# Optimization experiments

Measured on AMD Instinct MI355X. Metric: run time of the kernel, lower is better.

Reference implementation:

```python
import jax, jax.numpy as jnp
import numpy as np

FP8_E4M3_MAX = 448.0
FP4_E2M1_MAX = 6.0
BLOCK = 16  # NVFP4 block-scale granularity


def _round_e4m3(x):
    """Round non-negative values to fp8 e4m3 grid (3 mantissa bits, min normal 2^-6, max 448)."""
    a = jnp.abs(x)
    e = jnp.clip(jnp.floor(jnp.log2(jnp.where(a > 0, a, 1.0))), -6.0, 8.0)
    s = jnp.exp2(e)
    q = jnp.round(a / s * 8.0) / 8.0 * s
    q = jnp.clip(q, 0.0, FP8_E4M3_MAX)
    return jnp.where(a > 0, q, 0.0)


def _round_e2m1(x):
    """Round to fp4 e2m1 grid: +/- {0, 0.5, 1, 1.5, 2, 3, 4, 6}."""
    sgn = jnp.sign(x)
    a = jnp.clip(jnp.abs(x), 0.0, FP4_E2M1_MAX)
    e = jnp.clip(jnp.floor(jnp.log2(jnp.where(a > 0, a, 1.0))), 0.0, 2.0)
    step = jnp.exp2(e) * 0.5  # 0.5 in [0,2), 1 in [2,4), 2 in [4,6]
    q = jnp.round(a / step) * step
    return sgn * jnp.clip(q, 0.0, FP4_E2M1_MAX)


def quant_nvfp4(t):
    """Dynamic NVFP4 quantization (vLLM scaled_fp4_quant semantics).
    Returns (q_fp4 [R, K/16, 16], block_scale_e4m3 [R, K/16], global_scale []).
    Dequant: q * block_scale / global_scale."""
    gs = (FP8_E4M3_MAX * FP4_E2M1_MAX) / jnp.max(jnp.abs(t))
    tb = t.reshape(t.shape[0], -1, BLOCK)
    block_amax = jnp.max(jnp.abs(tb), axis=-1)              # [R, K/16]
    bs = _round_e4m3(block_amax / FP4_E2M1_MAX * gs)         # e4m3 block scales
    safe_bs = jnp.where(bs > 0, bs, 1.0)
    q = _round_e2m1(tb * (gs / safe_bs)[..., None])
    q = jnp.where((bs > 0)[..., None], q, 0.0)
    return q, bs, gs


def setup_inputs() -> dict:
    key = jax.random.key(0)
    kx, kw = jax.random.split(key)
    tokens, hidden = 8192, 4096
    x = jax.random.normal(kx, (tokens, 2 * hidden), dtype=jnp.float32)
    w = jax.random.uniform(kw, (hidden, hidden), dtype=jnp.float32)
    return {"x": x, "w": w}


def reference(x, w):
    d = x.shape[-1] // 2
    # SiluAndMul
    y = jax.nn.silu(x[..., :d]) * x[..., d:]                # [T, H]
    # dynamic NVFP4 quant of activation and weight
    qy, sy, gy = quant_nvfp4(y)
    qw, sw, gw = quant_nvfp4(w)
    # cutlass_scaled_fp4_mm: out = (qy*sy) @ (qw*sw)^T * alpha, alpha = 1/(gy*gw)
    a = (qy * sy[..., None]).reshape(y.shape)               # [T, H]
    b = (qw * sw[..., None]).reshape(w.shape)               # [H, H]
    alpha = 1.0 / (gy * gw)
    return (a @ b.T) * alpha
```

## Files before the change

### kernel.cpp

```cpp
#include <hip/hip_runtime.h>
#include <hip/hip_bf16.h>

typedef __attribute__((ext_vector_type(8))) short bf16x8;
typedef __attribute__((ext_vector_type(4))) float f32x4;


__device__ __forceinline__ float silu_mul_f(float a, float b) {
  float s = 1.0f / (1.0f + expf(-a));
  return (a * s) * b;
}

__device__ __forceinline__ int flog2(float a) {
  return (int)((__float_as_uint(a) >> 23) & 255u) - 127;
}
__device__ __forceinline__ float exp2i(int e) {
  return __uint_as_float((unsigned)(e + 127) << 23);
}

__device__ __forceinline__ float round_e4m3_f(float a) {
  if (!(a > 0.0f)) return 0.0f;
  int e = flog2(a);
  e = e < -6 ? -6 : (e > 8 ? 8 : e);
  float q = rintf(a * exp2i(3 - e)) * exp2i(e - 3);
  return fminf(q, 448.0f);
}

__device__ __forceinline__ float round_e2m1_f(float x) {
  float a = fminf(fabsf(x), 6.0f);
  if (!(a > 0.0f)) return 0.0f;
  int e = flog2(a);
  e = e < 0 ? 0 : (e > 2 ? 2 : e);
  float q = rintf(a * exp2i(1 - e)) * exp2i(e - 1);
  q = fminf(q, 6.0f);
  return (x < 0.0f) ? -q : q;
}

__global__ void init_scal_kernel(float* scal) {
  if (threadIdx.x < 2) scal[threadIdx.x] = 0.0f;
}


__global__ void amax2_kernel(const float* __restrict__ x, const float* __restrict__ w,
                             float* __restrict__ scal, long actU, long wU,
                             int hidden, int hqLog) {
  float mA = 0.0f, mW = 0.0f;
  const long stride = (long)gridDim.x * blockDim.x;
  const long hqm = (1L << hqLog) - 1;
  const long total = actU + wU;
  for (long u = (long)blockIdx.x * blockDim.x + threadIdx.x; u < total; u += stride) {
    if (u < actU) {
      long row = u >> hqLog;
      long c = u & hqm;
      const float* xr = x + ((row * (long)hidden) << 1);
      float4 v1 = ((const float4*)xr)[c];
      float4 v2 = ((const float4*)(xr + hidden))[c];
      mA = fmaxf(mA, fabsf(silu_mul_f(v1.x, v2.x)));
      mA = fmaxf(mA, fabsf(silu_mul_f(v1.y, v2.y)));
      mA = fmaxf(mA, fabsf(silu_mul_f(v1.z, v2.z)));
      mA = fmaxf(mA, fabsf(silu_mul_f(v1.w, v2.w)));
    } else {
      float4 v = ((const float4*)w)[u - actU];
      mW = fmaxf(mW, fmaxf(fmaxf(fabsf(v.x), fabsf(v.y)), fmaxf(fabsf(v.z), fabsf(v.w))));
    }
  }
#pragma unroll
  for (int off = 32; off > 0; off >>= 1) {
    mA = fmaxf(mA, __shfl_xor(mA, off));
    mW = fmaxf(mW, __shfl_xor(mW, off));
  }
  __shared__ float sA[4], sW[4];
  if ((threadIdx.x & 63) == 0) { sA[threadIdx.x >> 6] = mA; sW[threadIdx.x >> 6] = mW; }
  __syncthreads();
  if (threadIdx.x == 0) {
    atomicMax((unsigned int*)(scal + 0),
              __float_as_uint(fmaxf(fmaxf(sA[0], sA[1]), fmaxf(sA[2], sA[3]))));
    atomicMax((unsigned int*)(scal + 1),
              __float_as_uint(fmaxf(fmaxf(sW[0], sW[1]), fmaxf(sW[2], sW[3]))));
  }
}


__global__ void quant2_kernel(const float* __restrict__ x, const float* __restrict__ w,
                              __hip_bfloat16* __restrict__ A, __hip_bfloat16* __restrict__ B,
                              const float* __restrict__ scal, long actU, long wU,
                              int hidden, int hqLog) {
  const float gsA = 2688.0f / scal[0];
  const float gsW = 2688.0f / scal[1];
  const long stride = (long)gridDim.x * blockDim.x;
  const long hqm = (1L << hqLog) - 1;
  const long total = actU + wU;
  for (long u = (long)blockIdx.x * blockDim.x + threadIdx.x; u < total; u += stride) {
    float y0, y1, y2, y3, gs;
    unsigned short* dst;
    if (u < actU) {
      long row = u >> hqLog;
      long c = u & hqm;
      const float* xr = x + ((row * (long)hidden) << 1) + (c << 2);
      float4 v1 = *(const float4*)xr;
      float4 v2 = *(const float4*)(xr + hidden);
      y0 = silu_mul_f(v1.x, v2.x);
      y1 = silu_mul_f(v1.y, v2.y);
      y2 = silu_mul_f(v1.z, v2.z);
      y3 = silu_mul_f(v1.w, v2.w);
      gs = gsA;
      dst = (unsigned short*)A + (u << 2);
    } else {
      float4 v = ((const float4*)w)[u - actU];
      y0 = v.x; y1 = v.y; y2 = v.z; y3 = v.w;
      gs = gsW;
      dst = (unsigned short*)B + ((u - actU) << 2);
    }
    float lm = fmaxf(fmaxf(fabsf(y0), fabsf(y1)), fmaxf(fabsf(y2), fabsf(y3)));
    lm = fmaxf(lm, __shfl_xor(lm, 1));
    lm = fmaxf(lm, __shfl_xor(lm, 2));
    float bs = round_e4m3_f(lm / 6.0f * gs);
    float r = gs / (bs > 0.0f ? bs : 1.0f);
    ushort4 o;
    o.x = (unsigned short)(__float_as_uint(round_e2m1_f(y0 * r) * bs) >> 16);
    o.y = (unsigned short)(__float_as_uint(round_e2m1_f(y1 * r) * bs) >> 16);
    o.z = (unsigned short)(__float_as_uint(round_e2m1_f(y2 * r) * bs) >> 16);
    o.w = (unsigned short)(__float_as_uint(round_e2m1_f(y3 * r) * bs) >> 16);
    *(ushort4*)dst = o;
  }
}


__device__ __forceinline__ void gload_lds16(const void* g, void* l) {
  __builtin_amdgcn_global_load_lds(
      (const __attribute__((address_space(1))) void*)(uintptr_t)g,
      (__attribute__((address_space(3))) void*)(uintptr_t)l, 16, 0, 0);
}

template <unsigned IMM>
__device__ __forceinline__ bf16x8 lds_read16o(unsigned addr) {
  bf16x8 r;
  asm volatile("ds_read_b128 %0, %1 offset:%c2" : "=&v"(r) : "v"(addr), "i"(IMM));
  return r;
}

__device__ __forceinline__ f32x4 mfma_(bf16x8 a, bf16x8 b, f32x4 c) {
  return __builtin_amdgcn_mfma_f32_16x16x32_bf16(a, b, c, 0, 0, 0);
}

#define SP1 __builtin_amdgcn_s_setprio(1)
#define SP0 __builtin_amdgcn_s_setprio(0)
#define SCHEDB __builtin_amdgcn_sched_barrier(0)
#define WAITL(n) do { asm volatile("s_waitcnt lgkmcnt(" #n ")" ::: "memory"); SCHEDB; } while (0)
#define VMW4 do { asm volatile("s_waitcnt vmcnt(4)" ::: "memory"); } while (0)

#define STAGEA(PP, HH, KSB) do {                                        \
    const char* _s = pa + (KSB) + (HH) * 64;                            \
    gload_lds16(_s, ldsStA + (PP) * 32768 + (HH) * 16384);              \
    gload_lds16(_s + rowBig, ldsStA + (PP) * 32768 + (HH) * 16384 + 8192); } while (0)

#define STAGEB(PP, HH, KSB) do {                                        \
    const char* _s = pb + (KSB) + (HH) * 64;                            \
    gload_lds16(_s, ldsStB + (PP) * 32768 + (HH) * 16384);              \
    gload_lds16(_s + rowBig, ldsStB + (PP) * 32768 + (HH) * 16384 + 8192); } while (0)

#define RDA4(DST, PP, HH, MB) do {                                              \
    DST[0] = lds_read16o<(PP)*32768u + (HH)*16384u + ((MB)+0)*1024u>(vA);       \
    DST[1] = lds_read16o<(PP)*32768u + (HH)*16384u + ((MB)+1)*1024u>(vA);       \
    DST[2] = lds_read16o<(PP)*32768u + (HH)*16384u + ((MB)+2)*1024u>(vA);       \
    DST[3] = lds_read16o<(PP)*32768u + (HH)*16384u + ((MB)+3)*1024u>(vA); } while (0)

#define RDB4(DST, PP, HH) do {                                                  \
    DST[0] = lds_read16o<(PP)*32768u + (HH)*16384u + 0u>(vB);                   \
    DST[1] = lds_read16o<(PP)*32768u + (HH)*16384u + 1024u>(vB);                \
    DST[2] = lds_read16o<(PP)*32768u + (HH)*16384u + 2048u>(vB);                \
    DST[3] = lds_read16o<(PP)*32768u + (HH)*16384u + 3072u>(vB); } while (0)

#define MFMA16(AF, BF, MB) do {                                                  \
    acc[(MB)+0][0] = mfma_(AF[0], BF[0], acc[(MB)+0][0]);                        \
    acc[(MB)+1][0] = mfma_(AF[1], BF[0], acc[(MB)+1][0]);                        \
    acc[(MB)+2][0] = mfma_(AF[2], BF[0], acc[(MB)+2][0]);                        \
    acc[(MB)+3][0] = mfma_(AF[3], BF[0], acc[(MB)+3][0]);                        \
    acc[(MB)+0][1] = mfma_(AF[0], BF[1], acc[(MB)+0][1]);                        \
    acc[(MB)+1][1] = mfma_(AF[1], BF[1], acc[(MB)+1][1]);                        \
    acc[(MB)+2][1] = mfma_(AF[2], BF[1], acc[(MB)+2][1]);                        \
    acc[(MB)+3][1] = mfma_(AF[3], BF[1], acc[(MB)+3][1]);                        \
    acc[(MB)+0][2] = mfma_(AF[0], BF[2], acc[(MB)+0][2]);                        \
    acc[(MB)+1][2] = mfma_(AF[1], BF[2], acc[(MB)+1][2]);                        \
    acc[(MB)+2][2] = mfma_(AF[2], BF[2], acc[(MB)+2][2]);                        \
    acc[(MB)+3][2] = mfma_(AF[3], BF[2], acc[(MB)+3][2]);                        \
    acc[(MB)+0][3] = mfma_(AF[0], BF[3], acc[(MB)+0][3]);                        \
    acc[(MB)+1][3] = mfma_(AF[1], BF[3], acc[(MB)+1][3]);                        \
    acc[(MB)+2][3] = mfma_(AF[2], BF[3], acc[(MB)+2][3]);                        \
    acc[(MB)+3][3] = mfma_(AF[3], BF[3], acc[(MB)+3][3]); } while (0)

#define TILE(P, KSB) do {                                                        \
    STAGEA((P)^1, 0, KSB);                                                       \
    RDA4(aY, P, 0, 4);                                                           \
    WAITL(4);                                                                    \
    SP1; MFMA16(aX, bb0, 0); SP0;                                                \
    STAGEB((P)^1, 0, KSB);                                                       \
    VMW4;                                                                        \
    __builtin_amdgcn_s_barrier(); SCHEDB;                                        \
    RDA4(aX, P, 1, 0); RDB4(bb1, P, 1);                                          \
    WAITL(8);                                                                    \
    SP1; MFMA16(aY, bb0, 4); SP0;                                                \
    STAGEA((P)^1, 1, KSB);                                                       \
    RDA4(aY, P, 1, 4);                                                           \
    WAITL(4);                                                                    \
    SP1; MFMA16(aX, bb1, 0); SP0;                                                \
    STAGEB((P)^1, 1, KSB);                                                       \
    WAITL(0);                                                                    \
    VMW4;                                                                        \
    __builtin_amdgcn_s_barrier(); SCHEDB;                                        \
    RDA4(aX, (P)^1, 0, 0); RDB4(bb0, (P)^1, 0); SCHEDB;                          \
    SP1; MFMA16(aY, bb1, 4); SP0;                                                \
  } while (0)

__global__ __launch_bounds__(512, 2) void gemm_bt_kernel(
    const __hip_bfloat16* __restrict__ A, const __hip_bfloat16* __restrict__ B,
    float* __restrict__ C, const float* __restrict__ scal, int M, int N, int K) {
  __shared__ __align__(16) char lds[131072];

  const int nbm = M >> 8, nbn = N >> 8;
  int wg = blockIdx.x, bm, bn;
  if ((nbm & 7) == 0) {
    int band = nbm >> 3;
    int xcd = wg & 7, c = wg >> 3;
    bm = xcd * band + (c % band);
    bn = c / band;
  } else {
    bm = wg / nbn; bn = wg % nbn;
  }
  const int brow = bm << 8, bcol = bn << 8;

  const int tid = threadIdx.x;
  const int lane = tid & 63;
  const int wave = tid >> 6;
  const int wm = wave >> 2, wn = wave & 3;

  const int srow = tid >> 2;
  const int slc = (tid & 3) ^ ((tid >> 3) & 3);
  const char* pa = (const char*)(A + (size_t)(brow + srow) * K + slc * 8);
  const char* pb = (const char*)(B + (size_t)(bcol + srow) * K + slc * 8);
  const size_t rowBig = (size_t)128 * K * 2;
  char* ldsStA = lds + tid * 16;
  char* ldsStB = lds + 65536 + tid * 16;

  const unsigned ldsBase = (unsigned)(uintptr_t)lds;
  const unsigned xoff = (unsigned)((lane & 15) * 64) +
                        ((((unsigned)(lane >> 4)) ^ (((unsigned)lane >> 1) & 3u)) << 4);
  const unsigned vA = ldsBase + (unsigned)(wm * 8192) + xoff;
  const unsigned vB = ldsBase + 65536u + (unsigned)(wn * 4096) + xoff;

  f32x4 acc[8][4] = {};
  bf16x8 aX[4], aY[4], bb0[4], bb1[4];

  STAGEA(0, 0, 0); STAGEB(0, 0, 0); STAGEA(0, 1, 0); STAGEB(0, 1, 0);
  asm volatile("s_waitcnt vmcnt(0)" ::: "memory");
  __syncthreads();
  RDA4(aX, 0, 0, 0); RDB4(bb0, 0, 0); SCHEDB;

  const int nt = K >> 6;
  for (int it = 0; it < (nt >> 1); ++it) {
    int t0 = it << 1;
    int ks0 = (t0 + 1) * 128;
    int ks1 = (t0 + 2 == nt) ? 0 : (t0 + 2) * 128;
    TILE(0, ks0);
    TILE(1, ks1);
  }
  asm volatile("s_waitcnt lgkmcnt(0)" ::: "memory");
  asm volatile("s_waitcnt vmcnt(0)" ::: "memory");

  float gy = 2688.0f / scal[0];
  float gw = 2688.0f / scal[1];
  float alpha = 1.0f / (gy * gw);

#pragma unroll
  for (int m = 0; m < 8; ++m) {
    int rbase = brow + wm * 128 + m * 16 + ((lane >> 4) << 2);
#pragma unroll
    for (int n = 0; n < 4; ++n) {
      int col = bcol + wn * 64 + n * 16 + (lane & 15);
#pragma unroll
      for (int rg = 0; rg < 4; ++rg) {
        C[(size_t)(rbase + rg) * N + col] = acc[m][n][rg] * alpha;
      }
    }
  }
}


extern "C" void kernel_launch(void* const* d_in, const int* in_sizes, int n_in,
                              void* d_out, int out_size, void* d_ws, size_t ws_size,
                              hipStream_t stream) {
  const float* x = (const float*)d_in[0];
  const float* w = (const float*)d_in[1];
  float* out = (float*)d_out;

  int hidden = 1;
  while ((long long)hidden * hidden < (long long)in_sizes[1]) hidden <<= 1;
  int tokens = in_sizes[0] / (2 * hidden);

  char* ws = (char*)d_ws;
  __hip_bfloat16* Aq = (__hip_bfloat16*)ws;
  __hip_bfloat16* Bq = (__hip_bfloat16*)(ws + (size_t)tokens * hidden * 2);
  float* scal = (float*)(ws + (size_t)tokens * hidden * 2 + (size_t)hidden * hidden * 2);

  long actU = (long)tokens * hidden / 4;
  long wU = (long)hidden * hidden / 4;
  int hqLog = __builtin_ctz((unsigned)(hidden >> 2));

  init_scal_kernel<<<1, 64, 0, stream>>>(scal);
  amax2_kernel<<<2048, 256, 0, stream>>>(x, w, scal, actU, wU, hidden, hqLog);
  quant2_kernel<<<2048, 256, 0, stream>>>(x, w, Aq, Bq, scal, actU, wU, hidden, hqLog);

  int grid = (tokens >> 8) * (hidden >> 8);
  gemm_bt_kernel<<<grid, 512, 0, stream>>>(Aq, Bq, out, scal, tokens, hidden, hidden);
}
```

Measured before the change: 414.0 us.

## Switch GEMM to 32x32x16 MFMA and split quant kernels by tensor

The GEMM inner loop now uses 32x32x16 bf16 MFMA tiles with 16-float accumulators in place of 16x16x32. This halves the number of MFMA issues and LDS fragment reads per tile, with new swizzled LDS read addresses and a new epilogue layout. The amax and quant kernels now assign dedicated block ranges to activation and weight, which removes the per-element branch. Their loops are also unrolled by two to keep more loads in flight. The changed fragment addressing risks bank conflicts or wrong output layout if the swizzle math is off.

After: 395.5 us. 1.05x faster.

```diff
diff --git a/kernel.cpp b/kernel.cpp
--- a/kernel.cpp
+++ b/kernel.cpp
@@ -3,6 +3,7 @@
 
 typedef __attribute__((ext_vector_type(8))) short bf16x8;
 typedef __attribute__((ext_vector_type(4))) float f32x4;
+typedef __attribute__((ext_vector_type(16))) float f32x16;
 
 
 __device__ __forceinline__ float silu_mul_f(float a, float b) {
@@ -40,87 +41,125 @@
 }
 
 
+__device__ __forceinline__ float act_unit_max(const float* __restrict__ x, long u,
+                                              int hidden, long hqm, int hqLog) {
+  long row = u >> hqLog, c = u & hqm;
+  const float* xr = x + ((row * (long)hidden) << 1);
+  float4 v1 = ((const float4*)xr)[c];
+  float4 v2 = ((const float4*)(xr + hidden))[c];
+  float m = fmaxf(fabsf(silu_mul_f(v1.x, v2.x)), fabsf(silu_mul_f(v1.y, v2.y)));
+  m = fmaxf(m, fmaxf(fabsf(silu_mul_f(v1.z, v2.z)), fabsf(silu_mul_f(v1.w, v2.w))));
+  return m;
+}
+
 __global__ void amax2_kernel(const float* __restrict__ x, const float* __restrict__ w,
                              float* __restrict__ scal, long actU, long wU,
-                             int hidden, int hqLog) {
-  float mA = 0.0f, mW = 0.0f;
-  const long stride = (long)gridDim.x * blockDim.x;
+                             int hidden, int hqLog, int AB) {
   const long hqm = (1L << hqLog) - 1;
-  const long total = actU + wU;
-  for (long u = (long)blockIdx.x * blockDim.x + threadIdx.x; u < total; u += stride) {
-    if (u < actU) {
-      long row = u >> hqLog;
-      long c = u & hqm;
-      const float* xr = x + ((row * (long)hidden) << 1);
-      float4 v1 = ((const float4*)xr)[c];
-      float4 v2 = ((const float4*)(xr + hidden))[c];
-      mA = fmaxf(mA, fabsf(silu_mul_f(v1.x, v2.x)));
-      mA = fmaxf(mA, fabsf(silu_mul_f(v1.y, v2.y)));
-      mA = fmaxf(mA, fabsf(silu_mul_f(v1.z, v2.z)));
-      mA = fmaxf(mA, fabsf(silu_mul_f(v1.w, v2.w)));
-    } else {
-      float4 v = ((const float4*)w)[u - actU];
-      mW = fmaxf(mW, fmaxf(fmaxf(fabsf(v.x), fabsf(v.y)), fmaxf(fabsf(v.z), fabsf(v.w))));
-    }
-  }
-#pragma unroll
-  for (int off = 32; off > 0; off >>= 1) {
-    mA = fmaxf(mA, __shfl_xor(mA, off));
-    mW = fmaxf(mW, __shfl_xor(mW, off));
-  }
-  __shared__ float sA[4], sW[4];
-  if ((threadIdx.x & 63) == 0) { sA[threadIdx.x >> 6] = mA; sW[threadIdx.x >> 6] = mW; }
+  float m = 0.0f;
+  int which;
+  if ((int)blockIdx.x < AB) {
+    which = 0;
+    const long stride = (long)AB * blockDim.x;
+    long u = (long)blockIdx.x * blockDim.x + threadIdx.x;
+    for (; u + stride < actU; u += 2 * stride) {
+      float m0 = act_unit_max(x, u, hidden, hqm, hqLog);
+      float m1 = act_unit_max(x, u + stride, hidden, hqm, hqLog);
+      m = fmaxf(m, fmaxf(m0, m1));
+    }
+    if (u < actU) m = fmaxf(m, act_unit_max(x, u, hidden, hqm, hqLog));
+  } else {
+    which = 1;
+    const long stride = (long)(gridDim.x - AB) * blockDim.x;
+    long u = (long)((int)blockIdx.x - AB) * blockDim.x + threadIdx.x;
+    for (; u + stride < wU; u += 2 * stride) {
+      float4 v1 = ((const float4*)w)[u];
+      float4 v2 = ((const float4*)w)[u + stride];
+      float m0 = fmaxf(fmaxf(fabsf(v1.x), fabsf(v1.y)), fmaxf(fabsf(v1.z), fabsf(v1.w)));
+      float m1 = fmaxf(fmaxf(fabsf(v2.x), fabsf(v2.y)), fmaxf(fabsf(v2.z), fabsf(v2.w)));
+      m = fmaxf(m, fmaxf(m0, m1));
+    }
+    if (u < wU) {
+      float4 v = ((const float4*)w)[u];
+      m = fmaxf(m, fmaxf(fmaxf(fabsf(v.x), fabsf(v.y)), fmaxf(fabsf(v.z), fabsf(v.w))));
+    }
+  }
+#pragma unroll
+  for (int off = 32; off > 0; off >>= 1) m = fmaxf(m, __shfl_xor(m, off));
+  __shared__ float sm[4];
+  if ((threadIdx.x & 63) == 0) sm[threadIdx.x >> 6] = m;
   __syncthreads();
   if (threadIdx.x == 0) {
-    atomicMax((unsigned int*)(scal + 0),
-              __float_as_uint(fmaxf(fmaxf(sA[0], sA[1]), fmaxf(sA[2], sA[3]))));
-    atomicMax((unsigned int*)(scal + 1),
-              __float_as_uint(fmaxf(fmaxf(sW[0], sW[1]), fmaxf(sW[2], sW[3]))));
-  }
-}
-
+    float mm = fmaxf(fmaxf(sm[0], sm[1]), fmaxf(sm[2], sm[3]));
+    atomicMax((unsigned int*)(scal + which), __float_as_uint(mm));
+  }
+}
+
+
+__device__ __forceinline__ void quant_unit(float y0, float y1, float y2, float y3,
+                                           float gs, unsigned short* dst) {
+  float lm = fmaxf(fmaxf(fabsf(y0), fabsf(y1)), fmaxf(fabsf(y2), fabsf(y3)));
+  lm = fmaxf(lm, __shfl_xor(lm, 1));
+  lm = fmaxf(lm, __shfl_xor(lm, 2));
+  float bs = round_e4m3_f(lm / 6.0f * gs);
+  float r = gs / (bs > 0.0f ? bs : 1.0f);
+  ushort4 o;
+  o.x = (unsigned short)(__float_as_uint(round_e2m1_f(y0 * r) * bs) >> 16);
+  o.y = (unsigned short)(__float_as_uint(round_e2m1_f(y1 * r) * bs) >> 16);
+  o.z = (unsigned short)(__float_as_uint(round_e2m1_f(y2 * r) * bs) >> 16);
+  o.w = (unsigned short)(__float_as_uint(round_e2m1_f(y3 * r) * bs) >> 16);
+  *(ushort4*)dst = o;
+}
 
 __global__ void quant2_kernel(const float* __restrict__ x, const float* __restrict__ w,
                               __hip_bfloat16* __restrict__ A, __hip_bfloat16* __restrict__ B,
                               const float* __restrict__ scal, long actU, long wU,
-                              int hidden, int hqLog) {
-  const float gsA = 2688.0f / scal[0];
-  const float gsW = 2688.0f / scal[1];
-  const long stride = (long)gridDim.x * blockDim.x;
+                              int hidden, int hqLog, int AB) {
   const long hqm = (1L << hqLog) - 1;
-  const long total = actU + wU;
-  for (long u = (long)blockIdx.x * blockDim.x + threadIdx.x; u < total; u += stride) {
-    float y0, y1, y2, y3, gs;
-    unsigned short* dst;
+  if ((int)blockIdx.x < AB) {
+    const float gs = 2688.0f / scal[0];
+    const long stride = (long)AB * blockDim.x;
+    long u = (long)blockIdx.x * blockDim.x + threadIdx.x;
+    for (; u + stride < actU; u += 2 * stride) {
+      long ua = u, ub = u + stride;
+      long ra = ua >> hqLog, ca = ua & hqm;
+      long rb = ub >> hqLog, cb = ub & hqm;
+      const float* xa = x + ((ra * (long)hidden) << 1) + (ca << 2);
+      const float* xb = x + ((rb * (long)hidden) << 1) + (cb << 2);
+      float4 a1 = *(const float4*)xa;
+      float4 a2 = *(const float4*)(xa + hidden);
+      float4 b1 = *(const float4*)xb;
+      float4 b2 = *(const float4*)(xb + hidden);
+      quant_unit(silu_mul_f(a1.x, a2.x), silu_mul_f(a1.y, a2.y),
+                 silu_mul_f(a1.z, a2.z), silu_mul_f(a1.w, a2.w),
+                 gs, (unsigned short*)A + (ua << 2));
+      quant_unit(silu_mul_f(b1.x, b2.x), silu_mul_f(b1.y, b2.y),
+                 silu_mul_f(b1.z, b2.z), silu_mul_f(b1.w, b2.w),
+                 gs, (unsigned short*)A + (ub << 2));
+    }
     if (u < actU) {
-      long row = u >> hqLog;
       long c = u & hqm;
-      const float* xr = x + ((row * (long)hidden) << 1) + (c << 2);
-      float4 v1 = *(const float4*)xr;
-      float4 v2 = *(const float4*)(xr + hidden);
-      y0 = silu_mul_f(v1.x, v2.x);
-      y1 = silu_mul_f(v1.y, v2.y);
-      y2 = silu_mul_f(v1.z, v2.z);
-      y3 = silu_mul_f(v1.w, v2.w);
-      gs = gsA;
-      dst = (unsigned short*)A + (u << 2);
-    } else {
-      float4 v = ((const float4*)w)[u - actU];
-      y0 = v.x; y1 = v.y; y2 = v.z; y3 = v.w;
-      gs = gsW;
-      dst = (unsigned short*)B + ((u - actU) << 2);
-    }
-    float lm = fmaxf(fmaxf(fabsf(y0), fabsf(y1)), fmaxf(fabsf(y2), fabsf(y3)));
-    lm = fmaxf(lm, __shfl_xor(lm, 1));
-    lm = fmaxf(lm, __shfl_xor(lm, 2));
-    float bs = round_e4m3_f(lm / 6.0f * gs);
-    float r = gs / (bs > 0.0f ? bs : 1.0f);
-    ushort4 o;
-    o.x = (unsigned short)(__float_as_uint(round_e2m1_f(y0 * r) * bs) >> 16);
-    o.y = (unsigned short)(__float_as_uint(round_e2m1_f(y1 * r) * bs) >> 16);
-    o.z = (unsigned short)(__float_as_uint(round_e2m1_f(y2 * r) * bs) >> 16);
-    o.w = (unsigned short)(__float_as_uint(round_e2m1_f(y3 * r) * bs) >> 16);
-    *(ushort4*)dst = o;
+      const float* xa = x + (((u >> hqLog) * (long)hidden) << 1) + (c << 2);
+      float4 v1 = *(const float4*)xa;
+      float4 v2 = *(const float4*)(xa + hidden);
+      quant_unit(silu_mul_f(v1.x, v2.x), silu_mul_f(v1.y, v2.y),
+                 silu_mul_f(v1.z, v2.z), silu_mul_f(v1.w, v2.w),
+                 gs, (unsigned short*)A + (u << 2));
+    }
+  } else {
+    const float gs = 2688.0f / scal[1];
+    const long stride = (long)(gridDim.x - AB) * blockDim.x;
+    long u = (long)((int)blockIdx.x - AB) * blockDim.x + threadIdx.x;
+    for (; u + stride < wU; u += 2 * stride) {
+      float4 v1 = ((const float4*)w)[u];
+      float4 v2 = ((const float4*)w)[u + stride];
+      quant_unit(v1.x, v1.y, v1.z, v1.w, gs, (unsigned short*)B + (u << 2));
+      quant_unit(v2.x, v2.y, v2.z, v2.w, gs, (unsigned short*)B + ((u + stride) << 2));
+    }
+    if (u < wU) {
+      float4 v = ((const float4*)w)[u];
+      quant_unit(v.x, v.y, v.z, v.w, gs, (unsigned short*)B + (u << 2));
+    }
   }
 }
 
@@ -138,8 +177,8 @@
   return r;
 }
 
-__device__ __forceinline__ f32x4 mfma_(bf16x8 a, bf16x8 b, f32x4 c) {
-  return __builtin_amdgcn_mfma_f32_16x16x32_bf16(a, b, c, 0, 0, 0);
+__device__ __forceinline__ f32x16 mfma32(bf16x8 a, bf16x8 b, f32x16 c) {
+  return __builtin_amdgcn_mfma_f32_32x32x16_bf16(a, b, c, 0, 0, 0);
 }
 
 #define SP1 __builtin_amdgcn_s_setprio(1)
@@ -158,57 +197,47 @@
     gload_lds16(_s, ldsStB + (PP) * 32768 + (HH) * 16384);              \
     gload_lds16(_s + rowBig, ldsStB + (PP) * 32768 + (HH) * 16384 + 8192); } while (0)
 
-#define RDA4(DST, PP, HH, MB) do {                                              \
-    DST[0] = lds_read16o<(PP)*32768u + (HH)*16384u + ((MB)+0)*1024u>(vA);       \
-    DST[1] = lds_read16o<(PP)*32768u + (HH)*16384u + ((MB)+1)*1024u>(vA);       \
-    DST[2] = lds_read16o<(PP)*32768u + (HH)*16384u + ((MB)+2)*1024u>(vA);       \
-    DST[3] = lds_read16o<(PP)*32768u + (HH)*16384u + ((MB)+3)*1024u>(vA); } while (0)
-
-#define RDB4(DST, PP, HH) do {                                                  \
-    DST[0] = lds_read16o<(PP)*32768u + (HH)*16384u + 0u>(vB);                   \
-    DST[1] = lds_read16o<(PP)*32768u + (HH)*16384u + 1024u>(vB);                \
-    DST[2] = lds_read16o<(PP)*32768u + (HH)*16384u + 2048u>(vB);                \
-    DST[3] = lds_read16o<(PP)*32768u + (HH)*16384u + 3072u>(vB); } while (0)
-
-#define MFMA16(AF, BF, MB) do {                                                  \
-    acc[(MB)+0][0] = mfma_(AF[0], BF[0], acc[(MB)+0][0]);                        \
-    acc[(MB)+1][0] = mfma_(AF[1], BF[0], acc[(MB)+1][0]);                        \
-    acc[(MB)+2][0] = mfma_(AF[2], BF[0], acc[(MB)+2][0]);                        \
-    acc[(MB)+3][0] = mfma_(AF[3], BF[0], acc[(MB)+3][0]);                        \
-    acc[(MB)+0][1] = mfma_(AF[0], BF[1], acc[(MB)+0][1]);                        \
-    acc[(MB)+1][1] = mfma_(AF[1], BF[1], acc[(MB)+1][1]);                        \
-    acc[(MB)+2][1] = mfma_(AF[2], BF[1], acc[(MB)+2][1]);                        \
-    acc[(MB)+3][1] = mfma_(AF[3], BF[1], acc[(MB)+3][1]);                        \
-    acc[(MB)+0][2] = mfma_(AF[0], BF[2], acc[(MB)+0][2]);                        \
-    acc[(MB)+1][2] = mfma_(AF[1], BF[2], acc[(MB)+1][2]);                        \
-    acc[(MB)+2][2] = mfma_(AF[2], BF[2], acc[(MB)+2][2]);                        \
-    acc[(MB)+3][2] = mfma_(AF[3], BF[2], acc[(MB)+3][2]);                        \
-    acc[(MB)+0][3] = mfma_(AF[0], BF[3], acc[(MB)+0][3]);                        \
-    acc[(MB)+1][3] = mfma_(AF[1], BF[3], acc[(MB)+1][3]);                        \
-    acc[(MB)+2][3] = mfma_(AF[2], BF[3], acc[(MB)+2][3]);                        \
-    acc[(MB)+3][3] = mfma_(AF[3], BF[3], acc[(MB)+3][3]); } while (0)
-
-#define TILE(P, KSB) do {                                                        \
-    STAGEA((P)^1, 0, KSB);                                                       \
-    RDA4(aY, P, 0, 4);                                                           \
-    WAITL(4);                                                                    \
-    SP1; MFMA16(aX, bb0, 0); SP0;                                                \
-    STAGEB((P)^1, 0, KSB);                                                       \
-    VMW4;                                                                        \
-    __builtin_amdgcn_s_barrier(); SCHEDB;                                        \
-    RDA4(aX, P, 1, 0); RDB4(bb1, P, 1);                                          \
-    WAITL(8);                                                                    \
-    SP1; MFMA16(aY, bb0, 4); SP0;                                                \
-    STAGEA((P)^1, 1, KSB);                                                       \
-    RDA4(aY, P, 1, 4);                                                           \
-    WAITL(4);                                                                    \
-    SP1; MFMA16(aX, bb1, 0); SP0;                                                \
-    STAGEB((P)^1, 1, KSB);                                                       \
-    WAITL(0);                                                                    \
-    VMW4;                                                                        \
-    __builtin_amdgcn_s_barrier(); SCHEDB;                                        \
-    RDA4(aX, (P)^1, 0, 0); RDB4(bb0, (P)^1, 0); SCHEDB;                          \
-    SP1; MFMA16(aY, bb1, 4); SP0;                                                \
+#define RDA(DST, PP, HH, KS) do {                                           \
+    DST[0] = lds_read16o<(PP)*32768u + (HH)*16384u + 0u>(vA##KS);           \
+    DST[1] = lds_read16o<(PP)*32768u + (HH)*16384u + 2048u>(vA##KS);        \
+    DST[2] = lds_read16o<(PP)*32768u + (HH)*16384u + 4096u>(vA##KS);        \
+    DST[3] = lds_read16o<(PP)*32768u + (HH)*16384u + 6144u>(vA##KS); } while (0)
+
+#define RDB(DST, PP, HH, KS) do {                                           \
+    DST[0] = lds_read16o<(PP)*32768u + (HH)*16384u + 0u>(vB##KS);           \
+    DST[1] = lds_read16o<(PP)*32768u + (HH)*16384u + 2048u>(vB##KS); } while (0)
+
+#define MFMA8(AF, BF) do {                               \
+    acc[0][0] = mfma32(AF[0], BF[0], acc[0][0]);         \
+    acc[1][0] = mfma32(AF[1], BF[0], acc[1][0]);         \
+    acc[2][0] = mfma32(AF[2], BF[0], acc[2][0]);         \
+    acc[3][0] = mfma32(AF[3], BF[0], acc[3][0]);         \
+    acc[0][1] = mfma32(AF[0], BF[1], acc[0][1]);         \
+    acc[1][1] = mfma32(AF[1], BF[1], acc[1][1]);         \
+    acc[2][1] = mfma32(AF[2], BF[1], acc[2][1]);         \
+    acc[3][1] = mfma32(AF[3], BF[1], acc[3][1]); } while (0)
+
+#define TILE(P, KSB) do {                                                \
+    STAGEA((P)^1, 0, KSB);                                               \
+    RDA(aB, P, 0, 1); RDB(bB, P, 0, 1);                                  \
+    WAITL(6);                                                            \
+    SP1; MFMA8(aA, bA); SP0;                                             \
+    STAGEB((P)^1, 0, KSB);                                               \
+    VMW4;                                                                \
+    __builtin_amdgcn_s_barrier(); SCHEDB;                                \
+    RDA(aA, P, 1, 0); RDB(bA, P, 1, 0);                                  \
+    WAITL(6);                                                            \
+    SP1; MFMA8(aB, bB); SP0;                                             \
+    STAGEA((P)^1, 1, KSB);                                               \
+    RDA(aB, P, 1, 1); RDB(bB, P, 1, 1);                                  \
+    WAITL(6);                                                            \
+    SP1; MFMA8(aA, bA); SP0;                                             \
+    STAGEB((P)^1, 1, KSB);                                               \
+    VMW4;                                                                \
+    __builtin_amdgcn_s_barrier(); SCHEDB;                                \
+    RDA(aA, (P)^1, 0, 0); RDB(bA, (P)^1, 0, 0);                          \
+    WAITL(6);                                                            \
+    SP1; MFMA8(aB, bB); SP0;                                             \
   } while (0)
 
 __global__ __launch_bounds__(512, 2) void gemm_bt_kernel(
@@ -242,18 +271,22 @@
   char* ldsStB = lds + 65536 + tid * 16;
 
   const unsigned ldsBase = (unsigned)(uintptr_t)lds;
-  const unsigned xoff = (unsigned)((lane & 15) * 64) +
-                        ((((unsigned)(lane >> 4)) ^ (((unsigned)lane >> 1) & 3u)) << 4);
-  const unsigned vA = ldsBase + (unsigned)(wm * 8192) + xoff;
-  const unsigned vB = ldsBase + 65536u + (unsigned)(wn * 4096) + xoff;
-
-  f32x4 acc[8][4] = {};
-  bf16x8 aX[4], aY[4], bb0[4], bb1[4];
+  const unsigned l31 = (unsigned)(lane & 31);
+  const unsigned half = (unsigned)(lane >> 5);
+  const unsigned sw = ((unsigned)lane >> 1) & 3u;
+  const unsigned rbyte = l31 * 64u;
+  const unsigned vA0 = ldsBase + (unsigned)(wm * 8192) + rbyte + ((half ^ sw) << 4);
+  const unsigned vA1 = ldsBase + (unsigned)(wm * 8192) + rbyte + (((2u + half) ^ sw) << 4);
+  const unsigned vB0 = ldsBase + 65536u + (unsigned)(wn * 4096) + rbyte + ((half ^ sw) << 4);
+  const unsigned vB1 = ldsBase + 65536u + (unsigned)(wn * 4096) + rbyte + (((2u + half) ^ sw) << 4);
+
+  f32x16 acc[4][2] = {};
+  bf16x8 aA[4], aB[4], bA[2], bB[2];
 
   STAGEA(0, 0, 0); STAGEB(0, 0, 0); STAGEA(0, 1, 0); STAGEB(0, 1, 0);
   asm volatile("s_waitcnt vmcnt(0)" ::: "memory");
   __syncthreads();
-  RDA4(aX, 0, 0, 0); RDB4(bb0, 0, 0); SCHEDB;
+  RDA(aA, 0, 0, 0); RDB(bA, 0, 0, 0); SCHEDB;
 
   const int nt = K >> 6;
   for (int it = 0; it < (nt >> 1); ++it) {
@@ -271,14 +304,17 @@
   float alpha = 1.0f / (gy * gw);
 
 #pragma unroll
-  for (int m = 0; m < 8; ++m) {
-    int rbase = brow + wm * 128 + m * 16 + ((lane >> 4) << 2);
-#pragma unroll
-    for (int n = 0; n < 4; ++n) {
-      int col = bcol + wn * 64 + n * 16 + (lane & 15);
-#pragma unroll
-      for (int rg = 0; rg < 4; ++rg) {
-        C[(size_t)(rbase + rg) * N + col] = acc[m][n][rg] * alpha;
+  for (int mf = 0; mf < 4; ++mf) {
+    int rb = brow + wm * 128 + mf * 32 + (int)(half << 2);
+#pragma unroll
+    for (int nf = 0; nf < 2; ++nf) {
+      int col = bcol + wn * 64 + nf * 32 + (int)l31;
+#pragma unroll
+      for (int g = 0; g < 4; ++g) {
+#pragma unroll
+        for (int r = 0; r < 4; ++r) {
+          C[(size_t)(rb + 8 * g + r) * N + col] = acc[mf][nf][g * 4 + r] * alpha;
+        }
       }
     }
   }
@@ -304,10 +340,15 @@
   long actU = (long)tokens * hidden / 4;
   long wU = (long)hidden * hidden / 4;
   int hqLog = __builtin_ctz((unsigned)(hidden >> 2));
+  int nBlk = 2048;
+  int AB = (int)(((long)nBlk * actU) / (actU + wU));
+  AB &= ~3;
+  if (AB < 1) AB = 1;
+  if (AB > nBlk - 1) AB = nBlk - 1;
 
   init_scal_kernel<<<1, 64, 0, stream>>>(scal);
-  amax2_kernel<<<2048, 256, 0, stream>>>(x, w, scal, actU, wU, hidden, hqLog);
-  quant2_kernel<<<2048, 256, 0, stream>>>(x, w, Aq, Bq, scal, actU, wU, hidden, hqLog);
+  amax2_kernel<<<nBlk, 256, 0, stream>>>(x, w, scal, actU, wU, hidden, hqLog, AB);
+  quant2_kernel<<<nBlk, 256, 0, stream>>>(x, w, Aq, Bq, scal, actU, wU, hidden, hqLog, AB);
 
   int grid = (tokens >> 8) * (hidden >> 8);
   gemm_bt_kernel<<<grid, 512, 0, stream>>>(Aq, Bq, out, scal, tokens, hidden, hidden);
```
